# Kernel optimization log

Hardware: AMD Instinct MI355X
Metric: run time of the kernel (lower is better)

Reference implementation:

```python
import jax, jax.numpy as jnp
import numpy as np
from jax import lax

B, L, D_MODEL = 2, 4096, 1024
D_INNER = 2 * D_MODEL          # expand=2
D_STATE = D_INNER              # required: complex einsum contracts d_inner vs d_state
DT_RANK = 64                   # ceil(1024/16)
D_CONV = 4


def setup_inputs() -> dict:
    key = jax.random.key(0)
    ks = jax.random.split(key, 16)
    s = lambda *sh: 1.0 / np.sqrt(sh[-1])
    return {
        "hidden_states": jax.random.normal(ks[0], (B, L, D_MODEL), jnp.float32),
        "delta": jax.random.normal(ks[1], (B, L, DT_RANK), jnp.float32),
        # in_proj: Linear(d_model -> 2*d_inner), no bias
        "in_proj_w": jax.random.normal(ks[2], (2 * D_INNER, D_MODEL), jnp.float32) * s(D_MODEL),
        # depthwise causal conv1d: (out=d_inner, in/groups=1, k)
        "conv_w": jax.random.normal(ks[3], (D_INNER, 1, D_CONV), jnp.float32) * s(D_CONV),
        "conv_b": jax.random.normal(ks[4], (D_INNER,), jnp.float32) * 0.01,
        # ComplexStateSpace: only A_real affects the real output (x is real)
        "A_real": jax.random.normal(ks[5], (D_STATE, D_STATE), jnp.float32) * 0.1 / np.sqrt(D_STATE),
        # MIMO linears (torch Linear weight layout [out, in])
        "B_w": jax.random.normal(ks[6], (D_STATE, D_INNER), jnp.float32) * 0.1 * s(D_INNER),
        "C_w": jax.random.normal(ks[7], (D_INNER, D_STATE), jnp.float32) * 0.1 * s(D_STATE),
        "D_w": jax.random.normal(ks[8], (D_INNER, D_INNER), jnp.float32) * 0.1 * s(D_INNER),
        # SelectiveScan params
        "dt_proj_w": jax.random.normal(ks[9], (D_INNER, DT_RANK), jnp.float32) * 0.01,
        "dt_proj_b": jax.random.normal(ks[10], (D_INNER,), jnp.float32) * 0.01,
        "A_log": jax.random.uniform(ks[11], (D_INNER,), jnp.float32, -4.0, -1.0),
        "D_ss": jnp.ones((D_INNER,), jnp.float32),
        # out_proj: Linear(d_inner -> d_model), no bias
        "out_proj_w": jax.random.normal(ks[12], (D_MODEL, D_INNER), jnp.float32) * s(D_INNER),
    }


def reference(hidden_states, delta, in_proj_w, conv_w, conv_b, A_real,
              B_w, C_w, D_w, dt_proj_w, dt_proj_b, A_log, D_ss, out_proj_w):
    d_inner = A_log.shape[0]
    # in_proj + split
    xz = jnp.einsum('bld,ed->ble', hidden_states, in_proj_w)
    x, z = xz[..., :d_inner], xz[..., d_inner:]
    # depthwise causal conv1d (left-pad k-1 == torch pad both + truncate to L)
    xc = jnp.swapaxes(x, 1, 2)                      # [b, d, l]
    xc = lax.conv_general_dilated(xc, conv_w, window_strides=(1,),
                                  padding=[(D_CONV - 1, 0)],
                                  feature_group_count=d_inner)
    x = jnp.swapaxes(xc, 1, 2) + conv_b             # [b, l, d]
    x = jax.nn.silu(x)
    # ComplexStateSpace: real part of (x @ (A_real + iA_imag)) == x @ A_real
    x = x + jnp.einsum('bls,st->blt', x, A_real)
    # MIMO SSM: state_t = cumsum(B x)_t ; y_t = C state_t + D x_t  (vectorized)
    Bx = jnp.einsum('bld,sd->bls', x, B_w)          # [b, l, d_state]
    states = jnp.cumsum(Bx, axis=1)
    x_mimo = jnp.einsum('bls,es->ble', states, C_w) + jnp.einsum('bld,ed->ble', x, D_w)
    x = x + x_mimo
    # SelectiveScan: state = state * exp(dlt * A) + u, A = -exp(A_log)
    dlt = jax.nn.softplus(jnp.einsum('blr,dr->bld', delta, dt_proj_w) + dt_proj_b)
    decay = jnp.exp(dlt * (-jnp.exp(A_log)))        # [b, l, d], in (0, 1)

    def step(state, inp):
        dec, u = inp
        state = state * dec + u
        return state, state

    init = jnp.zeros_like(x[:, 0])
    _, scan_states = lax.scan(step, init,
                              (jnp.swapaxes(decay, 0, 1), jnp.swapaxes(x, 0, 1)))
    x = jnp.swapaxes(scan_states, 0, 1) + x * D_ss
    # gate + out projection
    out = x * jax.nn.silu(z)
    return jnp.einsum('ble,de->bld', out, out_proj_w)
```

## Files before the change

### kernel.cpp

```cpp
#include <hip/hip_runtime.h>
#include <cstdint>
#include <cstddef>


typedef unsigned short u16;
typedef __bf16 bf16x8 __attribute__((ext_vector_type(8)));
typedef float  f32x4  __attribute__((ext_vector_type(4)));

#define BDIM 256
#define M_ROWS 8192
#define LSEQ   4096
#define DI     2048
#define NCH    64
#define CLEN   64

__device__ __forceinline__ float bf2f(u16 h) {
    return __uint_as_float(((unsigned int)h) << 16);
}
__device__ __forceinline__ u16 f2bf(float f) {
    unsigned int u = __float_as_uint(f);
    u = u + 0x7fffu + ((u >> 16) & 1u);
    return (u16)(u >> 16);
}
__device__ __forceinline__ float siluf(float v) { return v / (1.0f + __expf(-v)); }

__device__ __forceinline__ void load16_to_lds(const u16* g, u16* l) {
    __builtin_amdgcn_global_load_lds((const __attribute__((address_space(1))) void*)g,
                                     (__attribute__((address_space(3))) void*)l,
                                     16, 0, 0);
}

__global__ void k_cvt_all(const float* __restrict__ hs, const float* __restrict__ inproj,
                          const float* __restrict__ Bw, const float* __restrict__ Cw,
                          const float* __restrict__ outw, const float* __restrict__ delta,
                          const float* __restrict__ dtw, const float* __restrict__ Areal,
                          const float* __restrict__ Dw, const float* __restrict__ Alog,
                          u16* __restrict__ XH, u16* __restrict__ W1, u16* __restrict__ WBb,
                          u16* __restrict__ WC, u16* __restrict__ WO, u16* __restrict__ DLT,
                          u16* __restrict__ WDT, u16* __restrict__ Pb, u16* __restrict__ Db,
                          float* __restrict__ NA) {
    long i = (long)(blockIdx.x * BDIM + threadIdx.x) * 4;
    if (i >= 32112640L) {
        long j = i - 32112640L;
        if (j < 2048) {
            float4 v = *reinterpret_cast<const float4*>(Alog + j);
            float4 o = {-__expf(v.x), -__expf(v.y), -__expf(v.z), -__expf(v.w)};
            *reinterpret_cast<float4*>(NA + j) = o;
        }
        return;
    }
    const float* src; u16* dst; long off; bool diag = false;
    if      (i <  8388608L) { src = hs;     dst = XH;  off = 0L; }
    else if (i < 12582912L) { src = inproj; dst = W1;  off = 8388608L; }
    else if (i < 16777216L) { src = Bw;     dst = WBb; off = 12582912L; }
    else if (i < 20971520L) { src = Cw;     dst = WC;  off = 16777216L; }
    else if (i < 23068672L) { src = outw;   dst = WO;  off = 20971520L; }
    else if (i < 23592960L) { src = delta;  dst = DLT; off = 23068672L; }
    else if (i < 23724032L) { src = dtw;    dst = WDT; off = 23592960L; }
    else if (i < 27918336L) { src = Areal;  dst = Pb;  off = 23724032L; diag = true; }
    else                    { src = Dw;     dst = Db;  off = 27918336L; diag = true; }
    long j = i - off;
    float4 v = *reinterpret_cast<const float4*>(src + j);
    if (diag) {
        int r = (int)(j >> 11), c = (int)(j & 2047);
        if (r >= c && r < c + 4) (&v.x)[r - c] += 1.0f;
    }
    ushort2 a = {f2bf(v.x), f2bf(v.y)};
    ushort2 b = {f2bf(v.z), f2bf(v.w)};
    *reinterpret_cast<ushort2*>(dst + j)     = a;
    *reinterpret_cast<ushort2*>(dst + j + 2) = b;
}

__device__ __forceinline__ void gemm_core(
    u16* As, u16* Bs,
    const u16* __restrict__ A1, const u16* __restrict__ W1, int K1,
    const u16* __restrict__ A2, const u16* __restrict__ W2, int K2,
    int N, float* __restrict__ outf, u16* __restrict__ outb, u16* __restrict__ outb2,
    const float* __restrict__ bias1, const float* __restrict__ bias2,
    int m0, int n0, int mode) {
    const int tid  = threadIdx.x;
    const int wave = tid >> 6;
    const int lane = tid & 63;
    const int wm = (wave >> 1) * 64;
    const int wn = (wave & 1) * 64;
    const int lr = lane & 15;
    const int lq = lane >> 4;
    const int stg_row = lane >> 3;
    const int stg_col = (((lane & 7) ^ (lane >> 3)) << 3);

    f32x4 acc[4][4] = {};

    const int nt1 = K1 >> 6;
    const int nt2 = K2 >> 6;
    const int ntot = nt1 + nt2;

    for (int kt = 0; kt < ntot; ++kt) {
        const u16* Ap; const u16* Wp; int ld, k0;
        if (kt < nt1) { Ap = A1; Wp = W1; ld = K1; k0 = kt << 6; }
        else          { Ap = A2; Wp = W2; ld = K2; k0 = (kt - nt1) << 6; }
        #pragma unroll
        for (int i = 0; i < 4; ++i) {
            int chunk = wave * 4 + i;
            int r = chunk * 8 + stg_row;
            load16_to_lds(Ap + (size_t)(m0 + r) * ld + (k0 + stg_col), As + chunk * 512);
            load16_to_lds(Wp + (size_t)(n0 + r) * ld + (k0 + stg_col), Bs + chunk * 512);
        }
        __syncthreads();
        #pragma unroll
        for (int kk = 0; kk < 64; kk += 32) {
            bf16x8 af[4], bfr[4];
            #pragma unroll
            for (int i = 0; i < 4; ++i) {
                int R = wm + i * 16 + lr;
                af[i] = *reinterpret_cast<const bf16x8*>(
                    &As[R * 64 + ((kk + lq * 8) ^ ((R & 7) << 3))]);
            }
            #pragma unroll
            for (int i = 0; i < 4; ++i) {
                int R = wn + i * 16 + lr;
                bfr[i] = *reinterpret_cast<const bf16x8*>(
                    &Bs[R * 64 + ((kk + lq * 8) ^ ((R & 7) << 3))]);
            }
            #pragma unroll
            for (int mi = 0; mi < 4; ++mi)
                #pragma unroll
                for (int ni = 0; ni < 4; ++ni)
                    acc[mi][ni] = __builtin_amdgcn_mfma_f32_16x16x32_bf16(
                        af[mi], bfr[ni], acc[mi][ni], 0, 0, 0);
        }
        __syncthreads();
    }

    if (mode == 8) {
        #pragma unroll
        for (int mi = 0; mi < 4; ++mi) {
            #pragma unroll
            for (int ni = 0; ni < 4; ++ni) {
                int row = m0 + wm + mi * 16 + lq * 4;
                int col = n0 + wn + ni * 16 + lr;
                ushort4 v;
                v.x = f2bf(acc[mi][ni][0]); v.y = f2bf(acc[mi][ni][1]);
                v.z = f2bf(acc[mi][ni][2]); v.w = f2bf(acc[mi][ni][3]);
                *reinterpret_cast<ushort4*>(outb + (size_t)col * 2048 + row) = v;
            }
        }
        return;
    }

    #pragma unroll
    for (int mi = 0; mi < 4; ++mi) {
        #pragma unroll
        for (int ni = 0; ni < 4; ++ni) {
            #pragma unroll
            for (int j = 0; j < 4; ++j) {
                int row = m0 + wm + mi * 16 + lq * 4 + j;
                int col = n0 + wn + ni * 16 + lr;
                float v = acc[mi][ni][j];
                if (mode == 6) {
                    if (col < 2048) outb [(size_t)row * 2048 + col]        = f2bf(v);
                    else            outb2[(size_t)row * 2048 + col - 2048] = f2bf(v);
                } else if (mode == 5) {
                    float dlt = v + bias1[col];
                    float sp  = (dlt > 15.f) ? dlt : __logf(1.f + __expf(dlt));
                    outb[(size_t)row * N + col] = f2bf(bias2[col] * sp);
                } else if (mode == 2) {
                    outf[(size_t)row * N + col] = v;
                } else {
                    outb[(size_t)row * N + col] = f2bf(v);
                }
            }
        }
    }
}

__device__ __forceinline__ void tile_coords(int q, int T, int gn, int& m0, int& n0) {
    int xcd  = q & 7;
    int loc  = q >> 3;
    int SM   = (T >> 3) / gn;
    int CH   = gn < 8 ? gn : 8;
    int span = SM * CH;
    int chunk = loc / span;
    int rem   = loc - chunk * span;
    int ml    = rem / CH;
    int nl    = rem - ml * CH;
    m0 = (xcd * SM + ml) * 128;
    n0 = (chunk * CH + nl) * 128;
}

__global__ __launch_bounds__(256, 4)
void k_batch1(const u16* __restrict__ XH, const u16* __restrict__ W1,
              const u16* __restrict__ WBb, const u16* __restrict__ Pb,
              const u16* __restrict__ Db,
              u16* __restrict__ PBt, u16* __restrict__ WXp,
              u16* __restrict__ XB, u16* __restrict__ ZB) {
    __shared__ u16 As[128 * 64];
    __shared__ u16 Bs[128 * 64];
    int bid = blockIdx.x;
    int m0, n0;
    if (bid < 256) {
        tile_coords(bid, 256, 16, m0, n0);
        gemm_core(As, Bs, Pb, WBb, DI, nullptr, nullptr, 0, DI,
                  nullptr, PBt, nullptr, nullptr, nullptr, m0, n0, 0);
    } else if (bid < 512) {
        tile_coords(bid - 256, 256, 16, m0, n0);
        gemm_core(As, Bs, Db, Pb, DI, nullptr, nullptr, 0, DI,
                  nullptr, WXp, nullptr, nullptr, nullptr, m0, n0, 0);
    } else {
        tile_coords(bid - 512, 2048, 32, m0, n0);
        gemm_core(As, Bs, XH, W1, 1024, nullptr, nullptr, 0, 4096,
                  nullptr, XB, ZB, nullptr, nullptr, m0, n0, 6);
    }
}

__global__ __launch_bounds__(256, 4)
void k_conv_pre3(const u16* __restrict__ x, const float* __restrict__ w,
                 const float* __restrict__ b, u16* __restrict__ out,
                 const u16* __restrict__ PBt, const u16* __restrict__ WC,
                 u16* __restrict__ WCBp) {
    __shared__ u16 As[128 * 64];
    __shared__ u16 Bs[128 * 64];
    if (blockIdx.x < 256) {
        int m0, n0;
        tile_coords(blockIdx.x, 256, 16, m0, n0);
        gemm_core(As, Bs, PBt, WC, DI, nullptr, nullptr, 0, DI,
                  nullptr, WCBp, nullptr, nullptr, nullptr, m0, n0, 8);
        return;
    }
    int idx = (blockIdx.x - 256) * BDIM + threadIdx.x;
    int d  = idx & (DI - 1);
    int bl = idx >> 11;
    int l  = bl & (LSEQ - 1);
    float4 wv = *reinterpret_cast<const float4*>(w + d * 4);
    float wj[4] = {wv.x, wv.y, wv.z, wv.w};
    float acc = b[d];
    #pragma unroll
    for (int j = 0; j < 4; ++j) {
        int ll = l - 3 + j;
        if (ll >= 0) acc += wj[j] * bf2f(x[(size_t)(bl - 3 + j) * DI + d]);
    }
    out[idx] = f2bf(siluf(acc));
}

__global__ __launch_bounds__(256, 4)
void k_batch36(const u16* __restrict__ XC, const u16* __restrict__ WCB2,
               const u16* __restrict__ DLT, const u16* __restrict__ WDT,
               const float* __restrict__ dtb, const float* __restrict__ NA,
               u16* __restrict__ BXC, u16* __restrict__ X3, u16* __restrict__ LD) {
    __shared__ u16 As[128 * 64];
    __shared__ u16 Bs[128 * 64];
    int bid = blockIdx.x;
    int g   = bid >> 3;
    int l8  = bid & 7;
    int t3  = g % 3;
    int m0, n0;
    if (t3 < 2) {
        int q = ((g / 3) * 2 + t3) * 8 + l8;
        tile_coords(q, 2048, 32, m0, n0);
        gemm_core(As, Bs, XC, WCB2, DI, nullptr, nullptr, 0, 4096,
                  nullptr, BXC, X3, nullptr, nullptr, m0, n0, 6);
    } else {
        int q = (g / 3) * 8 + l8;
        tile_coords(q, 1024, 16, m0, n0);
        gemm_core(As, Bs, DLT, WDT, 64, nullptr, nullptr, 0, DI,
                  nullptr, LD, nullptr, dtb, NA, m0, n0, 5);
    }
}

template <int MODE>
__global__ __launch_bounds__(256, 4)
void k_gemm(const u16* __restrict__ A1, const u16* __restrict__ W1, int K1,
            const u16* __restrict__ A2, const u16* __restrict__ W2, int K2,
            int N, float* __restrict__ outf, u16* __restrict__ outb) {
    __shared__ u16 As[128 * 64];
    __shared__ u16 Bs[128 * 64];
    int bid = blockIdx.x + gridDim.x * blockIdx.y;
    int m0, n0;
    tile_coords(bid, gridDim.x * gridDim.y, gridDim.x, m0, n0);
    gemm_core(As, Bs, A1, W1, K1, A2, W2, K2, N,
              outf, outb, nullptr, nullptr, nullptr, m0, n0, MODE);
}

__global__ void k_cumsum_p1(const u16* __restrict__ Bx, float* __restrict__ aux) {
    int t = blockIdx.x * BDIM + threadIdx.x;
    int s = t & (DI - 1);
    int c = (t >> 11) & (NCH - 1);
    int b = t >> 17;
    const u16* p = Bx + ((size_t)(b * LSEQ + c * CLEN) * DI) + s;
    float sum = 0.f;
    for (int i = 0; i < CLEN; ++i) sum += bf2f(p[(size_t)i * DI]);
    aux[t] = sum;
}
__global__ void k_cumsum_p23(const u16* __restrict__ Bx, const float* __restrict__ aux,
                             u16* x3) {
    int t = blockIdx.x * BDIM + threadIdx.x;
    int s = t & (DI - 1);
    int c = (t >> 11) & (NCH - 1);
    int b = t >> 17;
    float run = 0.f;
    for (int j = 0; j < c; ++j) run += aux[(b * NCH + j) * DI + s];
    size_t base = ((size_t)(b * LSEQ + c * CLEN) * DI) + s;
    for (int i = 0; i < CLEN; ++i) {
        size_t ix = base + (size_t)i * DI;
        run += bf2f(Bx[ix]);
        x3[ix] = f2bf(run + bf2f(x3[ix]));
    }
}

__global__ void k_scan_p1(const u16* __restrict__ ld_, const u16* __restrict__ u,
                          float* __restrict__ auxA, float* __restrict__ auxS) {
    int t = blockIdx.x * BDIM + threadIdx.x;
    int d = t & (DI - 1);
    int c = (t >> 11) & (NCH - 1);
    int b = t >> 17;
    size_t base = ((size_t)(b * LSEQ + c * CLEN) * DI) + d;
    float ap = 1.f, s = 0.f;
    for (int i = 0; i < CLEN; ++i) {
        size_t ix = base + (size_t)i * DI;
        float a = __expf(bf2f(ld_[ix]));
        s = fmaf(a, s, bf2f(u[ix]));
        ap *= a;
    }
    auxA[t] = ap; auxS[t] = s;
}
__global__ void k_scan_p23(const u16* __restrict__ ld_, const u16* __restrict__ u,
                           const float* __restrict__ auxA, const float* __restrict__ auxS,
                           const u16* __restrict__ z, const float* __restrict__ Dss,
                           u16* __restrict__ outb) {
    int t = blockIdx.x * BDIM + threadIdx.x;
    int d = t & (DI - 1);
    int c = (t >> 11) & (NCH - 1);
    int b = t >> 17;
    float s = 0.f;
    for (int j = 0; j < c; ++j) {
        int i = (b * NCH + j) * DI + d;
        s = fmaf(auxA[i], s, auxS[i]);
    }
    size_t base = ((size_t)(b * LSEQ + c * CLEN) * DI) + d;
    float dss = Dss[d];
    for (int i = 0; i < CLEN; ++i) {
        size_t ix = base + (size_t)i * DI;
        float a = __expf(bf2f(ld_[ix]));
        float uu = bf2f(u[ix]);
        s = fmaf(a, s, uu);
        float x4 = s + uu * dss;
        float zz = bf2f(z[ix]);
        outb[ix] = f2bf(x4 * siluf(zz));
    }
}

extern "C" void kernel_launch(void* const* d_in, const int* in_sizes, int n_in,
                              void* d_out, int out_size, void* d_ws, size_t ws_size,
                              hipStream_t stream) {
    const float* hs     = (const float*)d_in[0];
    const float* delta  = (const float*)d_in[1];
    const float* inproj = (const float*)d_in[2];
    const float* convw  = (const float*)d_in[3];
    const float* convb  = (const float*)d_in[4];
    const float* Areal  = (const float*)d_in[5];
    const float* Bw     = (const float*)d_in[6];
    const float* Cw     = (const float*)d_in[7];
    const float* Dw     = (const float*)d_in[8];
    const float* dtw    = (const float*)d_in[9];
    const float* dtb    = (const float*)d_in[10];
    const float* Alog   = (const float*)d_in[11];
    const float* Dss    = (const float*)d_in[12];
    const float* outw   = (const float*)d_in[13];
    float* out = (float*)d_out;

    const size_t SZ_ACT = (size_t)M_ROWS * DI * 2;
    char* p = (char*)d_ws;
    u16* ZB  = (u16*)p; p += SZ_ACT;
    u16* XB  = (u16*)p;
    u16* X3  = XB;      p += SZ_ACT;
    u16* XC  = (u16*)p;
    u16* OUT = XC;      p += SZ_ACT;
    u16* BXC = (u16*)p; p += SZ_ACT;
    u16* WCBp= (u16*)p;
    u16* WXp = WCBp + (size_t)DI * DI;
                        p += SZ_ACT;
    u16* XH  = (u16*)p;
    u16* LD  = XH;
                        p += (size_t)M_ROWS * 1024 * 2;
    u16* W1  = (u16*)p; p += (size_t)4096 * 1024 * 2;
    u16* WBb = (u16*)p; p += (size_t)DI * DI * 2;
    u16* WC  = (u16*)p; p += (size_t)DI * DI * 2;
    u16* Pb  = (u16*)p; p += (size_t)DI * DI * 2;
    u16* Db  = (u16*)p; p += (size_t)DI * DI * 2;
    u16* PBt = (u16*)p; p += (size_t)DI * DI * 2;
    p += (size_t)DI * DI * 2;
    u16* WO  = (u16*)p; p += (size_t)1024 * DI * 2;
    u16* WDT = (u16*)p; p += (size_t)DI * 64 * 2;
    u16* DLT = (u16*)p; p += (size_t)M_ROWS * 64 * 2;
    float* aux1 = (float*)p; p += (size_t)2 * NCH * DI * 4;
    float* auxA = (float*)p; p += (size_t)2 * NCH * DI * 4;
    float* auxS = (float*)p; p += (size_t)2 * NCH * DI * 4;
    float* NA   = (float*)p; p += (size_t)DI * 4;

    k_cvt_all<<<31362, BDIM, 0, stream>>>(hs, inproj, Bw, Cw, outw, delta, dtw,
                                          Areal, Dw, Alog,
                                          XH, W1, WBb, WC, WO, DLT, WDT, Pb, Db, NA);
    k_batch1<<<2560, BDIM, 0, stream>>>(XH, W1, WBb, Pb, Db, PBt, WXp, XB, ZB);
    k_conv_pre3<<<256 + (M_ROWS * DI) / BDIM, BDIM, 0, stream>>>(
        XB, convw, convb, XC, PBt, WC, WCBp);
    k_batch36<<<3072, BDIM, 0, stream>>>(XC, WCBp, DLT, WDT, dtb, NA, BXC, X3, LD);
    k_cumsum_p1<<<(2 * NCH * DI) / BDIM, BDIM, 0, stream>>>(BXC, aux1);
    k_cumsum_p23<<<(2 * NCH * DI) / BDIM, BDIM, 0, stream>>>(BXC, aux1, X3);
    k_scan_p1<<<(2 * NCH * DI) / BDIM, BDIM, 0, stream>>>(LD, X3, auxA, auxS);
    k_scan_p23<<<(2 * NCH * DI) / BDIM, BDIM, 0, stream>>>(LD, X3, auxA, auxS,
                                                           ZB, Dss, OUT);
    k_gemm<2><<<dim3(8, 64), BDIM, 0, stream>>>(OUT, WO, DI, nullptr, nullptr, 0,
                                                1024, out, nullptr);
}
```

Baseline: 636.4 us.

## Use 256x256-tile double-buffered GEMM for fused BX/X3 projection; move dt GEMM into conv kernel

Replaces the mixed batch36 kernel with a dedicated 512-thread GEMM using 256x256 tiles, double-buffered LDS staging, split-K-half MFMA issue with setprio, and an XCD-aware tile mapping for the 8192x4096x2048 projection. The small delta/dt_proj GEMM is moved into the conv kernel launch so it runs alongside the convolution. Larger tiles cut global/LDS traffic per FLOP, but they use much more LDS and registers per block, which lowers occupancy. Stores are done per element, which may be uncoalesced.

```diff
diff --git a/kernel.cpp b/kernel.cpp
--- a/kernel.cpp
+++ b/kernel.cpp
@@ -216,7 +216,10 @@
 void k_conv_pre3(const u16* __restrict__ x, const float* __restrict__ w,
                  const float* __restrict__ b, u16* __restrict__ out,
                  const u16* __restrict__ PBt, const u16* __restrict__ WC,
-                 u16* __restrict__ WCBp) {
+                 u16* __restrict__ WCBp,
+                 const u16* __restrict__ DLT, const u16* __restrict__ WDT,
+                 const float* __restrict__ dtb, const float* __restrict__ NA,
+                 u16* __restrict__ LD) {
     __shared__ u16 As[128 * 64];
     __shared__ u16 Bs[128 * 64];
     if (blockIdx.x < 256) {
@@ -226,7 +229,14 @@
                   nullptr, WCBp, nullptr, nullptr, nullptr, m0, n0, 8);
         return;
     }
-    int idx = (blockIdx.x - 256) * BDIM + threadIdx.x;
+    if (blockIdx.x < 1280) {
+        int m0, n0;
+        tile_coords(blockIdx.x - 256, 1024, 16, m0, n0);
+        gemm_core(As, Bs, DLT, WDT, 64, nullptr, nullptr, 0, DI,
+                  nullptr, LD, nullptr, dtb, NA, m0, n0, 5);
+        return;
+    }
+    int idx = (blockIdx.x - 1280) * BDIM + threadIdx.x;
     int d  = idx & (DI - 1);
     int bl = idx >> 11;
     int l  = bl & (LSEQ - 1);
@@ -241,29 +251,119 @@
     out[idx] = f2bf(siluf(acc));
 }
 
-__global__ __launch_bounds__(256, 4)
-void k_batch36(const u16* __restrict__ XC, const u16* __restrict__ WCB2,
-               const u16* __restrict__ DLT, const u16* __restrict__ WDT,
-               const float* __restrict__ dtb, const float* __restrict__ NA,
-               u16* __restrict__ BXC, u16* __restrict__ X3, u16* __restrict__ LD) {
-    __shared__ u16 As[128 * 64];
-    __shared__ u16 Bs[128 * 64];
-    int bid = blockIdx.x;
-    int g   = bid >> 3;
-    int l8  = bid & 7;
-    int t3  = g % 3;
-    int m0, n0;
-    if (t3 < 2) {
-        int q = ((g / 3) * 2 + t3) * 8 + l8;
-        tile_coords(q, 2048, 32, m0, n0);
-        gemm_core(As, Bs, XC, WCB2, DI, nullptr, nullptr, 0, 4096,
-                  nullptr, BXC, X3, nullptr, nullptr, m0, n0, 6);
-    } else {
-        int q = (g / 3) * 8 + l8;
-        tile_coords(q, 1024, 16, m0, n0);
-        gemm_core(As, Bs, DLT, WDT, 64, nullptr, nullptr, 0, DI,
-                  nullptr, LD, nullptr, dtb, NA, m0, n0, 5);
-    }
+__global__ __launch_bounds__(512, 2)
+void k_g36(const u16* __restrict__ A, const u16* __restrict__ W,
+           u16* __restrict__ BXC, u16* __restrict__ X3) {
+    __shared__ u16 As[2][256 * 64];
+    __shared__ u16 Bs[2][256 * 64];
+    const int tid  = threadIdx.x;
+    const int wave = tid >> 6;
+    const int lane = tid & 63;
+    const int wm = (wave >> 2) * 128;
+    const int wn = (wave & 3) * 64;
+    const int lr = lane & 15;
+    const int lq = lane >> 4;
+    const int stg_row = lane >> 3;
+    const int stg_col = (((lane & 7) ^ (lane >> 3)) << 3);
+
+    int q    = blockIdx.x;
+    int xcd  = q & 7;
+    int loc  = q >> 3;
+    int chnk = loc >> 5;
+    int rem  = loc & 31;
+    int ml   = rem >> 3, nl = rem & 7;
+    int m0 = (xcd * 4 + ml) * 256;
+    int n0 = (chnk * 8 + nl) * 256;
+
+    const int K = 2048;
+    const int nt = 32;
+
+    f32x4 acc[8][4] = {};
+
+    auto stage = [&](int kt) {
+        int c  = kt & 1;
+        int k0 = kt << 6;
+        #pragma unroll
+        for (int i = 0; i < 4; ++i) {
+            int ch = wave * 4 + i;
+            int r  = ch * 8 + stg_row;
+            load16_to_lds(A + (size_t)(m0 + r) * K + (k0 + stg_col), &As[c][ch * 512]);
+            load16_to_lds(W + (size_t)(n0 + r) * K + (k0 + stg_col), &Bs[c][ch * 512]);
+        }
+    };
+
+    stage(0);
+    stage(1);
+    asm volatile("s_waitcnt vmcnt(8)" ::: "memory");
+    __builtin_amdgcn_s_barrier();
+
+    for (int kt = 0; kt < nt; ++kt) {
+        const u16* as = As[kt & 1];
+        const u16* bs = Bs[kt & 1];
+        bf16x8 af[8], bfr[4];
+        #pragma unroll
+        for (int mi = 0; mi < 8; ++mi) {
+            int R = wm + mi * 16 + lr;
+            af[mi] = *reinterpret_cast<const bf16x8*>(
+                &as[R * 64 + ((lq * 8) ^ ((R & 7) << 3))]);
+        }
+        #pragma unroll
+        for (int ni = 0; ni < 4; ++ni) {
+            int R = wn + ni * 16 + lr;
+            bfr[ni] = *reinterpret_cast<const bf16x8*>(
+                &bs[R * 64 + ((lq * 8) ^ ((R & 7) << 3))]);
+        }
+        #pragma unroll
+        for (int mi = 0; mi < 8; ++mi)
+            #pragma unroll
+            for (int ni = 0; ni < 4; ++ni)
+                acc[mi][ni] = __builtin_amdgcn_mfma_f32_16x16x32_bf16(
+                    af[mi], bfr[ni], acc[mi][ni], 0, 0, 0);
+        bf16x8 af2[8], bfr2[4];
+        #pragma unroll
+        for (int mi = 0; mi < 8; ++mi) {
+            int R = wm + mi * 16 + lr;
+            af2[mi] = *reinterpret_cast<const bf16x8*>(
+                &as[R * 64 + ((32 + lq * 8) ^ ((R & 7) << 3))]);
+        }
+        #pragma unroll
+        for (int ni = 0; ni < 4; ++ni) {
+            int R = wn + ni * 16 + lr;
+            bfr2[ni] = *reinterpret_cast<const bf16x8*>(
+                &bs[R * 64 + ((32 + lq * 8) ^ ((R & 7) << 3))]);
+        }
+        asm volatile("s_waitcnt lgkmcnt(0)" ::: "memory");
+        __builtin_amdgcn_sched_barrier(0);
+        __builtin_amdgcn_s_barrier();
+        if (kt + 2 < nt) stage(kt + 2);
+        __builtin_amdgcn_s_setprio(1);
+        #pragma unroll
+        for (int mi = 0; mi < 8; ++mi)
+            #pragma unroll
+            for (int ni = 0; ni < 4; ++ni)
+                acc[mi][ni] = __builtin_amdgcn_mfma_f32_16x16x32_bf16(
+                    af2[mi], bfr2[ni], acc[mi][ni], 0, 0, 0);
+        __builtin_amdgcn_s_setprio(0);
+        if (kt + 2 < nt) {
+            asm volatile("s_waitcnt vmcnt(8)" ::: "memory");
+        } else if (kt + 1 < nt) {
+            asm volatile("s_waitcnt vmcnt(0)" ::: "memory");
+        }
+        __builtin_amdgcn_s_barrier();
+    }
+
+    u16* ob = (n0 < 2048) ? BXC : X3;
+    int nb  = n0 & 2047;
+    #pragma unroll
+    for (int mi = 0; mi < 8; ++mi)
+        #pragma unroll
+        for (int ni = 0; ni < 4; ++ni)
+            #pragma unroll
+            for (int j = 0; j < 4; ++j) {
+                int row = m0 + wm + mi * 16 + lq * 4 + j;
+                int col = nb + wn + ni * 16 + lr;
+                ob[(size_t)row * 2048 + col] = f2bf(acc[mi][ni][j]);
+            }
 }
 
 template <int MODE>
@@ -400,9 +500,9 @@
                                           Areal, Dw, Alog,
                                           XH, W1, WBb, WC, WO, DLT, WDT, Pb, Db, NA);
     k_batch1<<<2560, BDIM, 0, stream>>>(XH, W1, WBb, Pb, Db, PBt, WXp, XB, ZB);
-    k_conv_pre3<<<256 + (M_ROWS * DI) / BDIM, BDIM, 0, stream>>>(
-        XB, convw, convb, XC, PBt, WC, WCBp);
-    k_batch36<<<3072, BDIM, 0, stream>>>(XC, WCBp, DLT, WDT, dtb, NA, BXC, X3, LD);
+    k_conv_pre3<<<1280 + (M_ROWS * DI) / BDIM, BDIM, 0, stream>>>(
+        XB, convw, convb, XC, PBt, WC, WCBp, DLT, WDT, dtb, NA, LD);
+    k_g36<<<512, 512, 0, stream>>>(XC, WCBp, BXC, X3);
     k_cumsum_p1<<<(2 * NCH * DI) / BDIM, BDIM, 0, stream>>>(BXC, aux1);
     k_cumsum_p23<<<(2 * NCH * DI) / BDIM, BDIM, 0, stream>>>(BXC, aux1, X3);
     k_scan_p1<<<(2 * NCH * DI) / BDIM, BDIM, 0, stream>>>(LD, X3, auxA, auxS);
```

Measured after the change: 639.5 us. Within noise of the previous version (+0.5%).
